# Performance work log

Hardware: AMD Instinct MI355X
Metric: run time of the kernel (lower is better)

## Reference

```python
import jax, jax.numpy as jnp
import numpy as np

B, T, D = 64, 8, 512          # batch, num_tokens (= num_heads), hidden_size (= head_dim)
S = 512                       # history seq_len
NKV = 4                       # num_key_value_heads
G = T // NKV                  # num_key_value_groups
EPS = 1e-6
SCALE = D ** -0.5
NEG_INF = float('-inf')


def rmsnorm(x, w):
    # Qwen3NextRMSNorm: norm in fp32, scale by (1 + weight), cast back
    xf = x.astype(jnp.float32)
    n = xf * jax.lax.rsqrt(jnp.mean(xf * xf, axis=-1, keepdims=True) + EPS)
    return (n * (1.0 + w.astype(jnp.float32))).astype(x.dtype)


def setup_inputs() -> dict:
    key = jax.random.key(0)
    ks = jax.random.split(key, 8)
    return {
        'target_emb': jax.random.normal(ks[0], (B, T, D), dtype=jnp.float32),
        'history_emb': jax.random.normal(ks[1], (B, S, D), dtype=jnp.float32),
        'key_padding_mask': jax.random.bernoulli(ks[2], 0.2, (B, S)),
        'q_proj_w': jax.random.normal(ks[3], (D, D), dtype=jnp.float32) * (D ** -0.5),
        'k_proj_w': jax.random.normal(ks[4], (NKV * D, D), dtype=jnp.float32) * (D ** -0.5),
        'v_proj_w': jax.random.normal(ks[5], (NKV * D, D), dtype=jnp.float32) * (D ** -0.5),
        'q_norm_w': jnp.zeros((D,), dtype=jnp.float32),
        'k_norm_w': jnp.zeros((D,), dtype=jnp.float32),
    }


def reference(target_emb, history_emb, key_padding_mask,
              q_proj_w, k_proj_w, v_proj_w, q_norm_w, k_norm_w):
    # q_proj on flattened tokens: [B,T,D] @ W^T -> [B,T,D]
    q = jnp.einsum('btd,ed->bte', target_emb, q_proj_w)
    q = rmsnorm(q, q_norm_w)
    # k/v projections: [B,S,D] -> [B,S,NKV,D]
    k = jnp.einsum('bsd,ed->bse', history_emb, k_proj_w).reshape(B, S, NKV, D)
    v = jnp.einsum('bsd,ed->bse', history_emb, v_proj_w).reshape(B, S, NKV, D)
    k = rmsnorm(k, k_norm_w)
    # group queries by kv head instead of materializing repeat_kv copies
    qg = q.reshape(B, NKV, G, D)              # [B,NKV,G,D]
    kt = jnp.transpose(k, (0, 2, 1, 3))        # [B,NKV,S,D]
    vt = jnp.transpose(v, (0, 2, 1, 3))        # [B,NKV,S,D]
    scores = jnp.einsum('bngd,bnsd->bngs', qg, kt) * SCALE  # [B,NKV,G,S]
    bias = jnp.where(key_padding_mask, NEG_INF, 0.0).astype(jnp.float32)
    scores = scores + bias[:, None, None, :]
    attn = jax.nn.softmax(scores.astype(jnp.float32), axis=-1).astype(q.dtype)
    out = jnp.einsum('bngs,bnsd->bngd', attn, vt)  # [B,NKV,G,D]
    tokens = out.reshape(B, T, D)
    attn_weights = attn.reshape(B, T, 1, S)       # matches torch [B,H,1,S]
    return (tokens, attn_weights)
```

## Files before the change

kernel.cpp:

```cpp
#include <hip/hip_runtime.h>
#include <stdint.h>

#define NB 64
#define NT 8
#define ND 512
#define NS 512
#define NKV 4
#define BSLICE 32
#define NSLICE (NB / BSLICE)

typedef __attribute__((ext_vector_type(8))) short short8_t;
typedef __attribute__((ext_vector_type(8))) unsigned short ushort8_t;
typedef __attribute__((ext_vector_type(4))) float f32x4;

typedef const __attribute__((address_space(1))) void gas_void;
typedef __attribute__((address_space(3))) void las_void;

#define HSP_HI 0ull
#define WKH_B  16777216ull
#define WVH_B  18874368ull
#define WKT_B  20971520ull
#define THI_B  23068672ull
#define TLO_B  23592960ull
#define QWH_B  24117248ull
#define QWL_B  24641536ull
#define QP_B   25165824ull
#define DOT_B  26214400ull
#define OUTF_B 27262976ull
#define SSQ_B  28311552ull
#define PBUF_B 28966912ull
#define QPF_B  31064064ull
#define HH_B   33161216ull
#define HL_B   33685504ull
#define FLAG_B 34209792ull
#define ZERO_CNT 917504

__device__ __forceinline__ float b2f(unsigned short u) {
    union { unsigned int i; float f; } x; x.i = ((unsigned int)u) << 16; return x.f;
}
__device__ __forceinline__ unsigned short f2b(float f) {
    union { float f; unsigned int i; } x; x.f = f;
    unsigned int i = x.i;
    unsigned int r = i + 0x7FFFu + ((i >> 16) & 1u);
    return (unsigned short)(r >> 16);
}
__device__ __forceinline__ float in_elem(const void* p, long long i, int is_f32) {
    return is_f32 ? ((const float*)p)[i] : b2f(((const unsigned short*)p)[i]);
}
__device__ __forceinline__ void store_out(void* out, int is_f32, size_t idx, float v) {
    if (is_f32) ((float*)out)[idx] = v;
    else        ((unsigned short*)out)[idx] = f2b(v);
}

__global__ __launch_bounds__(256) void scan_zero_kernel(const unsigned short* __restrict__ hraw,
                                                        const void* __restrict__ mraw,
                                                        int* __restrict__ flag,
                                                        float* __restrict__ zbase) {
    const int tid = threadIdx.x;
    const int bx = blockIdx.x;
    if (bx >= 2) {
        zbase[(size_t)(bx - 2) * 256 + tid] = 0.0f;
        return;
    }
    if (bx == 0) {
        __shared__ int cnt;
        if (tid == 0) cnt = 0;
        __syncthreads();
        int c = 0;
#pragma unroll
        for (int it = 0; it < 16; ++it) {
            unsigned int e = (hraw[tid + it * 256] >> 7) & 0xFFu;
            if (e >= 0xF0u) ++c;
        }
        if (c) atomicAdd(&cnt, c);
        __syncthreads();
        if (tid == 0) flag[0] = (cnt >= 8) ? 1 : 0;
    } else {
        __shared__ int s_bf16, s_f32, s_not01, s_oddnz;
        if (tid == 0) { s_bf16 = 0; s_f32 = 0; s_not01 = 0; s_oddnz = 0; }
        __syncthreads();
        const unsigned int* w32 = (const unsigned int*)mraw;
        int f_bf16 = 0, f_f32 = 0, f_not01 = 0, f_oddnz = 0;
#pragma unroll
        for (int it = 0; it < 32; ++it) {
            const int i = tid + it * 256;
            unsigned int w = w32[i];
            if (w == 0x00003F80u || w == 0x3F803F80u) f_bf16 = 1;
            if (w == 0x3F800000u) f_f32 = 1;
            if (w != 0u && w != 1u && w != 0x3F800000u) f_not01 = 1;
            if ((i & 1) && w != 0u) f_oddnz = 1;
        }
        if (f_bf16)  s_bf16 = 1;
        if (f_f32)   s_f32 = 1;
        if (f_not01) s_not01 = 1;
        if (f_oddnz) s_oddnz = 1;
        __syncthreads();
        if (tid == 0) {
            int mode;
            if (s_bf16)       mode = 3;
            else if (s_f32)   mode = 0;
            else if (s_not01) mode = 1;
            else if (s_oddnz) mode = 0;
            else              mode = 2;
            flag[1] = mode;
        }
    }
}

__device__ __forceinline__ void split8(const void* src, long long i8, int is_f32,
                                       ushort8_t& h, ushort8_t& l) {
    if (is_f32) {
        const float* s = (const float*)src + i8;
        float4 a = *(const float4*)s;
        float4 b = *(const float4*)(s + 4);
        float v[8] = {a.x, a.y, a.z, a.w, b.x, b.y, b.z, b.w};
#pragma unroll
        for (int j = 0; j < 8; ++j) {
            unsigned short hh = f2b(v[j]);
            h[j] = hh;
            l[j] = f2b(v[j] - b2f(hh));
        }
    } else {
        h = *(const ushort8_t*)((const unsigned short*)src + i8);
#pragma unroll
        for (int j = 0; j < 8; ++j) l[j] = 0;
    }
}
__device__ __forceinline__ ushort8_t hi8(const void* src, long long i8, int is_f32) {
    ushort8_t h;
    if (is_f32) {
        const float* s = (const float*)src + i8;
        float4 a = *(const float4*)s;
        float4 b = *(const float4*)(s + 4);
        float v[8] = {a.x, a.y, a.z, a.w, b.x, b.y, b.z, b.w};
#pragma unroll
        for (int j = 0; j < 8; ++j) h[j] = f2b(v[j]);
    } else {
        h = *(const ushort8_t*)((const unsigned short*)src + i8);
    }
    return h;
}

__global__ __launch_bounds__(256) void prep_kernel(const void* __restrict__ target,
                                                   const void* __restrict__ Wq,
                                                   const void* __restrict__ Wk,
                                                   const void* __restrict__ Wv,
                                                   unsigned short* __restrict__ tHi,
                                                   unsigned short* __restrict__ tLo,
                                                   unsigned short* __restrict__ qwHi,
                                                   unsigned short* __restrict__ qwLo,
                                                   unsigned short* __restrict__ wkHi,
                                                   unsigned short* __restrict__ wvHi,
                                                   const int* __restrict__ flag) {
    const int bx = blockIdx.x;
    const int tid = threadIdx.x;
    const int is_f32 = flag[0];
    if (bx < 128) {
        const long long i8 = ((long long)bx * 256 + tid) * 8;
        ushort8_t h, l;
        split8(target, i8, is_f32, h, l);
        *(ushort8_t*)(tHi + i8) = h;
        *(ushort8_t*)(tLo + i8) = l;
    } else if (bx < 256) {
        const long long i8 = ((long long)(bx - 128) * 256 + tid) * 8;
        ushort8_t h, l;
        split8(Wq, i8, is_f32, h, l);
        *(ushort8_t*)(qwHi + i8) = h;
        *(ushort8_t*)(qwLo + i8) = l;
    } else if (bx < 768) {
        const long long i8 = ((long long)(bx - 256) * 256 + tid) * 8;
        *(ushort8_t*)(wkHi + i8) = hi8(Wk, i8, is_f32);
    } else {
        const long long i8 = ((long long)(bx - 768) * 256 + tid) * 8;
        *(ushort8_t*)(wvHi + i8) = hi8(Wv, i8, is_f32);
    }
}

__global__ __launch_bounds__(256) void presplit_hist_kernel(const void* __restrict__ src,
                                                            unsigned short* __restrict__ hi,
                                                            const int* __restrict__ flag,
                                                            long long elemOff) {
    const long long i8 = ((long long)blockIdx.x * 256 + threadIdx.x) * 8;
    *(ushort8_t*)(hi + i8) = hi8(src, elemOff + i8, flag[0]);
}


__device__ __forceinline__ void mfma2_tile(const unsigned short* __restrict__ Ah,
                                           const unsigned short* __restrict__ Al,
                                           const unsigned short* __restrict__ B,
                                           unsigned short* AsH, unsigned short* AsL,
                                           unsigned short* Bs,
                                           int m0, int n0, int tid,
                                           int ktBeg, int ktEnd,
                                           f32x4 acc[4][4]) {
    const int lane = tid & 63, wave = tid >> 6;
    const int wr = wave >> 1, wc = wave & 1;
    const int lr = lane & 15, lq = lane >> 4;
#pragma unroll
    for (int i = 0; i < 4; ++i)
#pragma unroll
        for (int j = 0; j < 4; ++j) acc[i][j] = (f32x4){0.f, 0.f, 0.f, 0.f};

    for (int kt = ktBeg; kt < ktEnd; ++kt) {
        const int k0 = kt << 5;
#pragma unroll
        for (int i = 0; i < 2; ++i) {
            const int c = i * 256 + tid;
            const size_t aoff = (size_t)(m0 + (c >> 2)) * 512 + (k0 + (c & 3) * 8);
            const size_t boff = (size_t)(n0 + (c >> 2)) * 512 + (k0 + (c & 3) * 8);
            __builtin_amdgcn_global_load_lds((gas_void*)(Ah + aoff), (las_void*)(AsH + c * 8), 16, 0, 0);
            __builtin_amdgcn_global_load_lds((gas_void*)(Al + aoff), (las_void*)(AsL + c * 8), 16, 0, 0);
            __builtin_amdgcn_global_load_lds((gas_void*)(B + boff), (las_void*)(Bs + c * 8), 16, 0, 0);
        }
        __syncthreads();
        short8_t aH[4], aL[4], bF[4];
#pragma unroll
        for (int t = 0; t < 4; ++t) {
            const int ao = (wr * 64 + t * 16 + lr) * 32 + lq * 8;
            aH[t] = *(const short8_t*)(AsH + ao);
            aL[t] = *(const short8_t*)(AsL + ao);
            bF[t] = *(const short8_t*)(Bs + (wc * 64 + t * 16 + lr) * 32 + lq * 8);
        }
#pragma unroll
        for (int ti = 0; ti < 4; ++ti)
#pragma unroll
            for (int tj = 0; tj < 4; ++tj)
                acc[ti][tj] = __builtin_amdgcn_mfma_f32_16x16x32_bf16(aH[ti], bF[tj], acc[ti][tj], 0, 0, 0);
#pragma unroll
        for (int ti = 0; ti < 4; ++ti)
#pragma unroll
            for (int tj = 0; tj < 4; ++tj)
                acc[ti][tj] = __builtin_amdgcn_mfma_f32_16x16x32_bf16(aL[ti], bF[tj], acc[ti][tj], 0, 0, 0);
        __syncthreads();
    }
}

__device__ __forceinline__ void mfma3_tile(const unsigned short* __restrict__ Ah,
                                           const unsigned short* __restrict__ Al,
                                           const unsigned short* __restrict__ Bh,
                                           const unsigned short* __restrict__ Bl,
                                           unsigned short* AsH, unsigned short* AsL,
                                           unsigned short* BsH, unsigned short* BsL,
                                           int m0, int n0, int tid,
                                           int ktBeg, int ktEnd,
                                           f32x4 acc[4][4]) {
    const int lane = tid & 63, wave = tid >> 6;
    const int wr = wave >> 1, wc = wave & 1;
    const int lr = lane & 15, lq = lane >> 4;
#pragma unroll
    for (int i = 0; i < 4; ++i)
#pragma unroll
        for (int j = 0; j < 4; ++j) acc[i][j] = (f32x4){0.f, 0.f, 0.f, 0.f};

    for (int kt = ktBeg; kt < ktEnd; ++kt) {
        const int k0 = kt << 5;
#pragma unroll
        for (int i = 0; i < 2; ++i) {
            const int c = i * 256 + tid;
            const size_t aoff = (size_t)(m0 + (c >> 2)) * 512 + (k0 + (c & 3) * 8);
            const size_t boff = (size_t)(n0 + (c >> 2)) * 512 + (k0 + (c & 3) * 8);
            __builtin_amdgcn_global_load_lds((gas_void*)(Ah + aoff), (las_void*)(AsH + c * 8), 16, 0, 0);
            __builtin_amdgcn_global_load_lds((gas_void*)(Al + aoff), (las_void*)(AsL + c * 8), 16, 0, 0);
            __builtin_amdgcn_global_load_lds((gas_void*)(Bh + boff), (las_void*)(BsH + c * 8), 16, 0, 0);
            __builtin_amdgcn_global_load_lds((gas_void*)(Bl + boff), (las_void*)(BsL + c * 8), 16, 0, 0);
        }
        __syncthreads();
        short8_t aH[4], aL[4], bH[4], bL[4];
#pragma unroll
        for (int t = 0; t < 4; ++t) {
            const int ao = (wr * 64 + t * 16 + lr) * 32 + lq * 8;
            const int bo = (wc * 64 + t * 16 + lr) * 32 + lq * 8;
            aH[t] = *(const short8_t*)(AsH + ao);
            aL[t] = *(const short8_t*)(AsL + ao);
            bH[t] = *(const short8_t*)(BsH + bo);
            bL[t] = *(const short8_t*)(BsL + bo);
        }
#pragma unroll
        for (int ti = 0; ti < 4; ++ti)
#pragma unroll
            for (int tj = 0; tj < 4; ++tj)
                acc[ti][tj] = __builtin_amdgcn_mfma_f32_16x16x32_bf16(aH[ti], bH[tj], acc[ti][tj], 0, 0, 0);
#pragma unroll
    for (int ti = 0; ti < 4; ++ti)
#pragma unroll
            for (int tj = 0; tj < 4; ++tj)
                acc[ti][tj] = __builtin_amdgcn_mfma_f32_16x16x32_bf16(aH[ti], bL[tj], acc[ti][tj], 0, 0, 0);
#pragma unroll
        for (int ti = 0; ti < 4; ++ti)
#pragma unroll
            for (int tj = 0; tj < 4; ++tj)
                acc[ti][tj] = __builtin_amdgcn_mfma_f32_16x16x32_bf16(aL[ti], bH[tj], acc[ti][tj], 0, 0, 0);
        __syncthreads();
    }
}

__global__ __launch_bounds__(256) void gemm3_ks(const unsigned short* __restrict__ Ah,
                                                const unsigned short* __restrict__ Al,
                                                const unsigned short* __restrict__ Bh,
                                                const unsigned short* __restrict__ Bl,
                                                float* __restrict__ C) {
    __shared__ __align__(16) unsigned short AsH[128 * 32];
    __shared__ __align__(16) unsigned short AsL[128 * 32];
    __shared__ __align__(16) unsigned short BsH[128 * 32];
    __shared__ __align__(16) unsigned short BsL[128 * 32];
    const int m0 = blockIdx.x * 128, n0 = blockIdx.y * 128;
    const int kt0 = blockIdx.z * 4;
    const int tid = threadIdx.x;
    f32x4 acc[4][4];
    mfma3_tile(Ah, Al, Bh, Bl, AsH, AsL, BsH, BsL, m0, n0, tid, kt0, kt0 + 4, acc);
    const int lane = tid & 63, wave = tid >> 6;
    const int wr = wave >> 1, wc = wave & 1;
    const int lr = lane & 15, lq = lane >> 4;
#pragma unroll
    for (int ti = 0; ti < 4; ++ti)
#pragma unroll
        for (int tj = 0; tj < 4; ++tj)
#pragma unroll
            for (int r = 0; r < 4; ++r) {
                const int row = m0 + wr * 64 + ti * 16 + lq * 4 + r;
                const int col = n0 + wc * 64 + tj * 16 + lr;
                atomicAdd(&C[(size_t)row * 512 + col], acc[ti][tj][r]);
            }
}

__global__ __launch_bounds__(64) void rmsnorm_qperm(const float* __restrict__ q,
                                                    const void* __restrict__ qnw,
                                                    const void* __restrict__ knw,
                                                    float* __restrict__ qpF,
                                                    const int* __restrict__ flag) {
    const int row = blockIdx.x;
    const int lane = threadIdx.x;
    const int is_f32 = flag[0];
    const float* p = q + (size_t)row * ND + lane * 8;
    float v[8];
    float4 a = *(const float4*)p;
    float4 b4 = *(const float4*)(p + 4);
    v[0] = a.x; v[1] = a.y; v[2] = a.z; v[3] = a.w;
    v[4] = b4.x; v[5] = b4.y; v[6] = b4.z; v[7] = b4.w;
    float ssq = 0.f;
#pragma unroll
    for (int j = 0; j < 8; ++j) ssq = fmaf(v[j], v[j], ssq);
#pragma unroll
    for (int off = 1; off < 64; off <<= 1) ssq += __shfl_xor(ssq, off);
    float r = rsqrtf(ssq * (1.0f / ND) + 1e-6f);
    const float SCALE = 0.044194173824159216f;
    const int b = row >> 3, h = row & 7;
    const int prow = (h >> 1) * 128 + b * 2 + (h & 1);
    float o[8];
#pragma unroll
    for (int j = 0; j < 8; ++j) {
        int e = lane * 8 + j;
        o[j] = v[j] * r * (1.0f + in_elem(qnw, e, is_f32)) * (1.0f + in_elem(knw, e, is_f32)) * SCALE;
    }
    float4* dst = (float4*)(qpF + (size_t)prow * 512 + lane * 8);
    dst[0] = (float4){o[0], o[1], o[2], o[3]};
    dst[1] = (float4){o[4], o[5], o[6], o[7]};
}

#define SSQ8_ABUF(b) ((b) * 32768)
#define SSQ8_BBUF(b) (65536 + (b) * 32768)
#define EPI_STRIDE 136

#define SSQ8_STAGE_A(r, tt, bufOff)                                                       \
    do {                                                                                  \
        const int rcA0_ = rl0 + (r) * 64;                                                 \
        __builtin_amdgcn_global_load_lds(                                                 \
            (gas_void*)(A + (size_t)(mBase + rcA0_) * 512 + (tt) * 64 + ksw),             \
            (las_void*)(smem + (bufOff) + rcA0_ * 128 + k0 * 2), 16, 0, 0);               \
        const int rcA1_ = rcA0_ + 128;                                                    \
        __builtin_amdgcn_global_load_lds(                                                 \
            (gas_void*)(A + (size_t)(mBase + rcA1_) * 512 + (tt) * 64 + ksw),             \
            (las_void*)(smem + (bufOff) + rcA1_ * 128 + k0 * 2), 16, 0, 0);               \
    } while (0)

#define SSQ8_STAGE_B(q, tt, bufOff)                                                       \
    do {                                                                                  \
        const int rcB0_ = bR + (q) * 32;                                                  \
        __builtin_amdgcn_global_load_lds(                                                 \
            (gas_void*)(W + (size_t)(nBase + rcB0_) * 512 + (tt) * 64 + ksw),             \
            (las_void*)(smem + (bufOff) + rcB0_ * 128 + k0 * 2), 16, 0, 0);               \
        const int rcB1_ = rcB0_ + 128;                                                    \
        __builtin_amdgcn_global_load_lds(                                                 \
            (gas_void*)(W + (size_t)(nBase + rcB1_) * 512 + (tt) * 64 + ksw),             \
            (las_void*)(smem + (bufOff) + rcB1_ * 128 + k0 * 2), 16, 0, 0);               \
    } while (0)

#define SSQ8_READ_A(qm, bufOff)                                                           \
    _Pragma("unroll")                                                                     \
    for (int m_ = 0; m_ < 4; ++m_) {                                                      \
        const int rc_ = wm * 128 + (qm) * 64 + m_ * 16 + lr;                              \
        af[m_][0] = *(const short8_t*)(smem + (bufOff) + rc_ * 128 + kb0);                \
        af[m_][1] = *(const short8_t*)(smem + (bufOff) + rc_ * 128 + kb1);                \
    }

#define SSQ8_READ_B2(nh, bufOff)                                                          \
    _Pragma("unroll")                                                                     \
    for (int n_ = 0; n_ < 2; ++n_) {                                                      \
        const int cc_ = wn * 64 + (nh) * 32 + n_ * 16 + lr;                               \
        bf[(nh) * 2 + n_][0] = *(const short8_t*)(smem + (bufOff) + cc_ * 128 + kb0);     \
        bf[(nh) * 2 + n_][1] = *(const short8_t*)(smem + (bufOff) + cc_ * 128 + kb1);     \
    }

#define SSQ8_MFMA_Q(qm, nh)                                                               \
    _Pragma("unroll")                                                                     \
    for (int m_ = 0; m_ < 4; ++m_)                                                        \
    _Pragma("unroll")                                                                     \
    for (int n_ = 0; n_ < 2; ++n_) {                                                      \
        acc[(qm) * 4 + m_][(nh) * 2 + n_] = __builtin_amdgcn_mfma_f32_16x16x32_bf16(      \
            af[m_][0], bf[(nh) * 2 + n_][0], acc[(qm) * 4 + m_][(nh) * 2 + n_], 0, 0, 0); \
        acc[(qm) * 4 + m_][(nh) * 2 + n_] = __builtin_amdgcn_mfma_f32_16x16x32_bf16(      \
            af[m_][1], bf[(nh) * 2 + n_][1], acc[(qm) * 4 + m_][(nh) * 2 + n_], 0, 0, 0); \
    }

#define SSQ8_SYNC_PRE()                                                                   \
    __builtin_amdgcn_s_barrier();                                                         \
    asm volatile("s_waitcnt lgkmcnt(0)" ::: "memory");                                    \
    __builtin_amdgcn_sched_barrier(0);                                                    \
    __builtin_amdgcn_s_setprio(1);

#define SSQ8_SYNC_POST()                                                                  \
    __builtin_amdgcn_s_setprio(0);                                                        \
    __builtin_amdgcn_s_barrier();

__global__ __launch_bounds__(512) void gemm_ssq8(const unsigned short* __restrict__ A,
                                                 const unsigned short* __restrict__ W,
                                                 const float* __restrict__ qpF,
                                                 float* __restrict__ ssq,
                                                 float* __restrict__ dotb,
                                                 int b0) {
    extern __shared__ char smem[];
    const int tid = threadIdx.x;
    const int lane = tid & 63, wave = tid >> 6;
    const int wm = wave >> 2, wn = wave & 3;
    const int lr = lane & 15, lq = lane >> 4;
    const int mBase = blockIdx.x * 256;
    const int nBase = blockIdx.y * 256;

    const int rl0 = tid >> 3;
    const int k0 = (tid & 7) << 3;
    const int ksw = k0 ^ ((rl0 & 7) << 3);
    const int bR = (rl0 & 31) | ((rl0 >> 5) << 6);

    const int kb0 = ((lq * 8) ^ ((lr & 7) << 3)) * 2;
    const int kb1 = ((32 + lq * 8) ^ ((lr & 7) << 3)) * 2;

    f32x4 acc[8][4];
#pragma unroll
    for (int i = 0; i < 8; ++i)
#pragma unroll
        for (int j = 0; j < 4; ++j) acc[i][j] = (f32x4){0.f, 0.f, 0.f, 0.f};

    SSQ8_STAGE_A(0, 0, SSQ8_ABUF(0));
    SSQ8_STAGE_B(0, 0, SSQ8_BBUF(0));
    SSQ8_STAGE_A(1, 0, SSQ8_ABUF(0));
    SSQ8_STAGE_B(1, 0, SSQ8_BBUF(0));
    SSQ8_STAGE_A(0, 1, SSQ8_ABUF(1));
    SSQ8_STAGE_B(0, 1, SSQ8_BBUF(1));
    asm volatile("s_waitcnt vmcnt(4)" ::: "memory");
    __builtin_amdgcn_s_barrier();

    short8_t af[4][2], bf[4][2];

#pragma unroll
    for (int t = 0; t < 8; ++t) {
        const int cur = t & 1, nxt = cur ^ 1;
        const int aC = SSQ8_ABUF(cur), bC = SSQ8_BBUF(cur);
        const int aN = SSQ8_ABUF(nxt), bN = SSQ8_BBUF(nxt);
        SSQ8_READ_A(0, aC)
        SSQ8_READ_B2(0, bC)
        if (t + 1 < 8) SSQ8_STAGE_A(1, t + 1, aN);
        SSQ8_SYNC_PRE()
        SSQ8_MFMA_Q(0, 0)
        SSQ8_SYNC_POST()
        SSQ8_READ_B2(1, bC)
        if (t + 1 < 8) SSQ8_STAGE_B(1, t + 1, bN);
        SSQ8_SYNC_PRE()
        SSQ8_MFMA_Q(0, 1)
        SSQ8_SYNC_POST()
        SSQ8_READ_A(1, aC)
        if (t + 2 < 8) SSQ8_STAGE_A(0, t + 2, aC);
        SSQ8_SYNC_PRE()
        SSQ8_MFMA_Q(1, 0)
        SSQ8_SYNC_POST()
        if (t + 2 < 8) SSQ8_STAGE_B(0, t + 2, bC);
        __builtin_amdgcn_s_barrier();
        __builtin_amdgcn_sched_barrier(0);
        __builtin_amdgcn_s_setprio(1);
        SSQ8_MFMA_Q(1, 1)
        __builtin_amdgcn_s_setprio(0);
        if (t < 6) {
            asm volatile("s_waitcnt vmcnt(4)" ::: "memory");
        } else if (t == 6) {
            asm volatile("s_waitcnt vmcnt(0)" ::: "memory");
        }
        __builtin_amdgcn_s_barrier();
    }

    const int nh = (int)(blockIdx.y >> 1);
    const int bG = b0 + (mBase >> 9);
    const int bn = bG * 4 + nh;
    const int sBase0 = mBase & 511;
    const int dBase = (nBase & 511) + wn * 64 + lr;
    const size_t qrow0 = (size_t)(nh * 128 + bG * 2) * 512;
    float qv0[4], qv1[4];
#pragma unroll
    for (int n = 0; n < 4; ++n) {
        qv0[n] = qpF[qrow0 + dBase + n * 16];
        qv1[n] = qpF[qrow0 + 512 + dBase + n * 16];
    }
    float* lv   = (float*)smem;
    float* ld0  = lv  + 64 * EPI_STRIDE;
    float* ld1  = ld0 + 64 * EPI_STRIDE;
    float* part = ld1 + 64 * EPI_STRIDE;
    const int col = wn * 16 + lr;

#pragma unroll
    for (int p = 0; p < 2; ++p) {
        __syncthreads();
#pragma unroll
        for (int mm = 0; mm < 4; ++mm) {
            const int m = p * 4 + mm;
            f32x4 vv, dd0, dd1;
#pragma unroll
            for (int r = 0; r < 4; ++r) {
                float v = 0.f, d0 = 0.f, d1 = 0.f;
#pragma unroll
                for (int n = 0; n < 4; ++n) {
                    float x = acc[m][n][r];
                    v = fmaf(x, x, v);
                    d0 = fmaf(x, qv0[n], d0);
                    d1 = fmaf(x, qv1[n], d1);
                }
                vv[r] = v; dd0[r] = d0; dd1[r] = d1;
            }
            const int idx = wm * 64 + mm * 16 + lq * 4;
            *(f32x4*)(lv  + col * EPI_STRIDE + idx) = vv;
            *(f32x4*)(ld0 + col * EPI_STRIDE + idx) = dd0;
            *(f32x4*)(ld1 + col * EPI_STRIDE + idx) = dd1;
        }
        __syncthreads();
        {
            const int t = tid >> 7, i = tid & 127;
            float s0 = 0.f, s1 = 0.f, s2 = 0.f;
#pragma unroll
            for (int c = 0; c < 16; ++c) {
                const int cc = t * 16 + c;
                s0 += lv [cc * EPI_STRIDE + i];
                s1 += ld0[cc * EPI_STRIDE + i];
                s2 += ld1[cc * EPI_STRIDE + i];
            }
            part[(0 * 128 + i) * 4 + t] = s0;
            part[(1 * 128 + i) * 4 + t] = s1;
            part[(2 * 128 + i) * 4 + t] = s2;
        }
        __syncthreads();
        if (tid < 384) {
            const int v = tid >> 7, i = tid & 127;
            f32x4 pp = *(const f32x4*)(part + ((size_t)v * 128 + i) * 4);
            float sum = (pp[0] + pp[1]) + (pp[2] + pp[3]);
            const int s = sBase0 + (i >> 6) * 128 + p * 64 + (i & 63);
            if (v == 0)      atomicAdd(&ssq[(size_t)bn * 512 + s], sum);
            else if (v == 1) atomicAdd(&dotb[((size_t)bn * 2 + 0) * 512 + s], sum);
            else             atomicAdd(&dotb[((size_t)bn * 2 + 1) * 512 + s], sum);
        }
    }
}

__global__ __launch_bounds__(512) void softmax_slice(const float* __restrict__ ssq,
                                                     const float* __restrict__ dot,
                                                     const void* __restrict__ mraw,
                                                     float* __restrict__ pbuf,
                                                     void* __restrict__ out,
                                                     const int* __restrict__ flag,
                                                     int b0) {
    const int bn = b0 * 4 + blockIdx.x;
    const int b = bn >> 2;
    const int tid = threadIdx.x;
    const int wave = tid >> 6, lane = tid & 63;
    const int is_f32 = flag[0];
    const int mode = flag[1];
    __shared__ float red[32];

    float sq = ssq[(size_t)bn * 512 + tid];
    float rms = rsqrtf(sq * (1.0f / ND) + 1e-6f);
    const int mi = b * NS + tid;
    int masked;
    if (mode == 3)      masked = (((const unsigned short*)mraw)[mi] != 0);
    else if (mode == 1) masked = (((const unsigned char*)mraw)[mi] != 0);
    else if (mode == 0) masked = (((const unsigned int*)mraw)[mi] != 0u);
    else                masked = (((const unsigned int*)mraw)[2 * mi] != 0u);
    float ninf = -__builtin_inff();
    float v0 = masked ? ninf : dot[((size_t)bn * 2 + 0) * 512 + tid] * rms;
    float v1 = masked ? ninf : dot[((size_t)bn * 2 + 1) * 512 + tid] * rms;

    float m0 = v0, m1 = v1;
#pragma unroll
    for (int off = 1; off < 64; off <<= 1) {
        m0 = fmaxf(m0, __shfl_xor(m0, off));
        m1 = fmaxf(m1, __shfl_xor(m1, off));
    }
    if (lane == 0) { red[wave] = m0; red[8 + wave] = m1; }
    __syncthreads();
    m0 = red[0]; m1 = red[8];
#pragma unroll
    for (int w = 1; w < 8; ++w) { m0 = fmaxf(m0, red[w]); m1 = fmaxf(m1, red[8 + w]); }
    float e0 = __expf(v0 - m0), e1 = __expf(v1 - m1);
    float su0 = e0, su1 = e1;
#pragma unroll
    for (int off = 1; off < 64; off <<= 1) {
        su0 += __shfl_xor(su0, off);
        su1 += __shfl_xor(su1, off);
    }
    if (lane == 0) { red[16 + wave] = su0; red[24 + wave] = su1; }
    __syncthreads();
    float t0 = 0.f, t1 = 0.f;
#pragma unroll
    for (int w = 0; w < 8; ++w) { t0 += red[16 + w]; t1 += red[24 + w]; }
    float p0 = e0 / t0, p1 = e1 / t1;

    pbuf[((size_t)bn * 2 + 0) * 512 + tid] = p0;
    pbuf[((size_t)bn * 2 + 1) * 512 + tid] = p1;
    size_t abase = 262144u + (size_t)bn * 1024 + tid;
    store_out(out, is_f32, abase, p0);
    store_out(out, is_f32, abase + 512, p1);
}

__global__ __launch_bounds__(512) void htilde_kernel(const unsigned short* __restrict__ hspHi,
                                                     const float* __restrict__ pbuf,
                                                     unsigned short* __restrict__ hHi,
                                                     unsigned short* __restrict__ hLo,
                                                     int b0) {
    __shared__ float pl[8][512];
    __shared__ float red[8][64][8];
    const int bl = blockIdx.x;
    const int bG = b0 + bl;
    const int d0 = blockIdx.y * 64;
    const int tid = threadIdx.x;
#pragma unroll
    for (int k = 0; k < 8; ++k) {
        const int j = tid + k * 512;
        const int h = j >> 9, s = j & 511;
        pl[h][s] = pbuf[((size_t)(bG * 4 + (h >> 1)) * 2 + (h & 1)) * 512 + s];
    }
    __syncthreads();

    const int dl = tid & 63, sl = tid >> 6;
    const unsigned short* hb = hspHi + (size_t)bl * 512 * 512 + d0 + dl;
    float acc[8];
#pragma unroll
    for (int h = 0; h < 8; ++h) acc[h] = 0.f;
#pragma unroll 4
    for (int i = 0; i < 64; ++i) {
        const int s = i * 8 + sl;
        float hv = b2f(hb[(size_t)s * 512]);
#pragma unroll
        for (int h = 0; h < 8; ++h) acc[h] = fmaf(pl[h][s], hv, acc[h]);
    }
#pragma unroll
    for (int h = 0; h < 8; ++h) red[sl][dl][h] = acc[h];
    __syncthreads();

    const int dl2 = tid >> 3, h2 = tid & 7;
    float v = 0.f;
#pragma unroll
    for (int s2 = 0; s2 < 8; ++s2) v += red[s2][dl2][h2];
    const int row = (h2 >> 1) * 128 + bG * 2 + (h2 & 1);
    unsigned short hv = f2b(v);
    hHi[(size_t)row * 512 + d0 + dl2] = hv;
    hLo[(size_t)row * 512 + d0 + dl2] = f2b(v - b2f(hv));
}

__global__ __launch_bounds__(256) void gemm_out_ks(const unsigned short* __restrict__ hHi,
                                                   const unsigned short* __restrict__ hLo,
                                                   const unsigned short* __restrict__ wvHi,
                                                   float* __restrict__ outF) {
    __shared__ __align__(16) unsigned short AsH[128 * 32];
    __shared__ __align__(16) unsigned short AsL[128 * 32];
    __shared__ __align__(16) unsigned short Bs[128 * 32];
    const int n = blockIdx.x;
    const int m0 = n * 128, n0 = blockIdx.y * 128;
    const int kt0 = blockIdx.z * 4;
    const int tid = threadIdx.x;
    f32x4 acc[4][4];
    mfma2_tile(hHi, hLo, wvHi + (size_t)n * 512 * 512, AsH, AsL, Bs, m0, n0, tid, kt0, kt0 + 4, acc);

    const int lane = tid & 63, wave = tid >> 6;
    const int wr = wave >> 1, wc = wave & 1;
    const int lr = lane & 15, lq = lane >> 4;
#pragma unroll
    for (int ti = 0; ti < 4; ++ti)
#pragma unroll
        for (int tj = 0; tj < 4; ++tj)
#pragma unroll
            for (int r = 0; r < 4; ++r) {
                const int row = m0 + wr * 64 + ti * 16 + lq * 4 + r;
                const int e = n0 + wc * 64 + tj * 16 + lr;
                atomicAdd(&outF[(size_t)row * 512 + e], acc[ti][tj][r]);
            }
}

__global__ __launch_bounds__(256) void out_final_kernel(const float* __restrict__ outF,
                                                        void* __restrict__ out,
                                                        const int* __restrict__ flag) {
    const size_t i = (size_t)blockIdx.x * 256 + threadIdx.x;
    const int row = (int)(i >> 9), e = (int)(i & 511);
    const int n = row >> 7, rl = row & 127;
    const int b = rl >> 1, g = rl & 1;
    store_out(out, flag[0], (size_t)(b * 8 + n * 2 + g) * 512 + e, outF[i]);
}

extern "C" void kernel_launch(void* const* d_in, const int* in_sizes, int n_in,
                              void* d_out, int out_size, void* d_ws, size_t ws_size,
                              hipStream_t stream) {
    (void)in_sizes; (void)n_in; (void)out_size; (void)ws_size;
    const void* target = d_in[0];
    const void* hist   = d_in[1];
    const void* mraw   = d_in[2];
    const void* Wq     = d_in[3];
    const void* Wk     = d_in[4];
    const void* Wv     = d_in[5];
    const void* qnw    = d_in[6];
    const void* knw    = d_in[7];

    char* w = (char*)d_ws;
    unsigned short* hspHi = (unsigned short*)(w + HSP_HI);
    unsigned short* wkHi  = (unsigned short*)(w + WKH_B);
    unsigned short* wvHi  = (unsigned short*)(w + WVH_B);
    unsigned short* tHi   = (unsigned short*)(w + THI_B);
    unsigned short* tLo   = (unsigned short*)(w + TLO_B);
    unsigned short* qwHi  = (unsigned short*)(w + QWH_B);
    unsigned short* qwLo  = (unsigned short*)(w + QWL_B);
    float* qp    = (float*)(w + QP_B);
    float* dotb  = (float*)(w + DOT_B);
    float* outF  = (float*)(w + OUTF_B);
    float* ssq   = (float*)(w + SSQ_B);
    float* pbuf  = (float*)(w + PBUF_B);
    float* qpF   = (float*)(w + QPF_B);
    unsigned short* hHi  = (unsigned short*)(w + HH_B);
    unsigned short* hLo  = (unsigned short*)(w + HL_B);
    int* flag = (int*)(w + FLAG_B);

    static bool attr_set = false;
    if (!attr_set) {
        (void)hipFuncSetAttribute(reinterpret_cast<const void*>(&gemm_ssq8),
                                  hipFuncAttributeMaxDynamicSharedMemorySize, 131072);
        attr_set = true;
    }

    scan_zero_kernel<<<2 + ZERO_CNT / 256, 256, 0, stream>>>(
        (const unsigned short*)hist, mraw, flag, qp);
    prep_kernel<<<1280, 256, 0, stream>>>(target, Wq, Wk, Wv, tHi, tLo, qwHi, qwLo,
                                          wkHi, wvHi, flag);

    gemm3_ks<<<dim3(4, 4, 4), 256, 0, stream>>>(tHi, tLo, qwHi, qwLo, qp);
    rmsnorm_qperm<<<NB * NT, 64, 0, stream>>>(qp, qnw, knw, qpF, flag);

    for (int sl = 0; sl < NSLICE; ++sl) {
        const int b0 = sl * BSLICE;
        presplit_hist_kernel<<<4096, 256, 0, stream>>>(hist, hspHi, flag,
                                                       (long long)sl * BSLICE * 512 * 512);
        gemm_ssq8<<<dim3(64, 8), 512, 131072, stream>>>(hspHi, wkHi, qpF, ssq, dotb, b0);
        softmax_slice<<<BSLICE * NKV, 512, 0, stream>>>(ssq, dotb, mraw, pbuf, d_out, flag, b0);
        htilde_kernel<<<dim3(BSLICE, 8), 512, 0, stream>>>(hspHi, pbuf, hHi, hLo, b0);
    }
    gemm_out_ks<<<dim3(4, 4, 4), 256, 0, stream>>>(hHi, hLo, wvHi, outF);
    out_final_kernel<<<1024, 256, 0, stream>>>(outF, d_out, flag);
}
```

Before: 244.7 us.

## Fuse history bf16 conversion into GEMM A-staging and htilde loads

Removes the separate presplit_hist kernel that converted history embeddings to bf16 in workspace. The GEMM now loads fp32 (or bf16) history directly into registers, converts it, and writes it to LDS through a software-pipelined register stage in place of direct global-to-LDS loads. htilde reads the raw fp32 history directly. This saves one kernel launch per slice and a write plus re-read of the bf16 copy. In exchange the GEMM reads twice the bytes for A, uses more registers, and its load pipeline and waitcnt accounting become more complex.

```diff
diff --git a/kernel.cpp b/kernel.cpp
--- a/kernel.cpp
+++ b/kernel.cpp
@@ -176,14 +176,6 @@
     }
 }
 
-__global__ __launch_bounds__(256) void presplit_hist_kernel(const void* __restrict__ src,
-                                                            unsigned short* __restrict__ hi,
-                                                            const int* __restrict__ flag,
-                                                            long long elemOff) {
-    const long long i8 = ((long long)blockIdx.x * 256 + threadIdx.x) * 8;
-    *(ushort8_t*)(hi + i8) = hi8(src, elemOff + i8, flag[0]);
-}
-
 
 __device__ __forceinline__ void mfma2_tile(const unsigned short* __restrict__ Ah,
                                            const unsigned short* __restrict__ Al,
@@ -361,16 +353,31 @@
 #define SSQ8_BBUF(b) (65536 + (b) * 32768)
 #define EPI_STRIDE 136
 
-#define SSQ8_STAGE_A(r, tt, bufOff)                                                       \
+#define SSQA_ISSUE(r0, r1, tt, F, U)                                                      \
     do {                                                                                  \
-        const int rcA0_ = rl0 + (r) * 64;                                                 \
-        __builtin_amdgcn_global_load_lds(                                                 \
-            (gas_void*)(A + (size_t)(mBase + rcA0_) * 512 + (tt) * 64 + ksw),             \
-            (las_void*)(smem + (bufOff) + rcA0_ * 128 + k0 * 2), 16, 0, 0);               \
-        const int rcA1_ = rcA0_ + 128;                                                    \
-        __builtin_amdgcn_global_load_lds(                                                 \
-            (gas_void*)(A + (size_t)(mBase + rcA1_) * 512 + (tt) * 64 + ksw),             \
-            (las_void*)(smem + (bufOff) + rcA1_ * 128 + k0 * 2), 16, 0, 0);               \
+        const size_t ke_ = (size_t)(tt) * 64 + ksw;                                       \
+        if (is_f32) {                                                                     \
+            F[0] = *(const float4*)(histF + (size_t)(mBase + (r0)) * 512 + ke_);          \
+            F[1] = *(const float4*)(histF + (size_t)(mBase + (r0)) * 512 + ke_ + 4);      \
+            F[2] = *(const float4*)(histF + (size_t)(mBase + (r1)) * 512 + ke_);          \
+            F[3] = *(const float4*)(histF + (size_t)(mBase + (r1)) * 512 + ke_ + 4);      \
+        } else {                                                                          \
+            U[0] = *(const ushort8_t*)(histU + (size_t)(mBase + (r0)) * 512 + ke_);       \
+            U[1] = *(const ushort8_t*)(histU + (size_t)(mBase + (r1)) * 512 + ke_);       \
+        }                                                                                 \
+    } while (0)
+
+#define SSQA_WRITE(r0, r1, bufOff, F, U)                                                  \
+    do {                                                                                  \
+        ushort8_t w0_, w1_;                                                               \
+        if (is_f32) {                                                                     \
+            float v0_[8] = {F[0].x, F[0].y, F[0].z, F[0].w, F[1].x, F[1].y, F[1].z, F[1].w}; \
+            float v1_[8] = {F[2].x, F[2].y, F[2].z, F[2].w, F[3].x, F[3].y, F[3].z, F[3].w}; \
+            _Pragma("unroll")                                                             \
+            for (int j_ = 0; j_ < 8; ++j_) { w0_[j_] = (short)f2b(v0_[j_]); w1_[j_] = (short)f2b(v1_[j_]); } \
+        } else { w0_ = (ushort8_t)U[0]; w1_ = (ushort8_t)U[1]; }                          \
+        *(ushort8_t*)(smem + (bufOff) + (r0) * 128 + k0 * 2) = w0_;                       \
+        *(ushort8_t*)(smem + (bufOff) + (r1) * 128 + k0 * 2) = w1_;                       \
     } while (0)
 
 #define SSQ8_STAGE_B(q, tt, bufOff)                                                       \
@@ -422,11 +429,12 @@
     __builtin_amdgcn_s_setprio(0);                                                        \
     __builtin_amdgcn_s_barrier();
 
-__global__ __launch_bounds__(512) void gemm_ssq8(const unsigned short* __restrict__ A,
+__global__ __launch_bounds__(512) void gemm_ssq8(const void* __restrict__ hist,
                                                  const unsigned short* __restrict__ W,
                                                  const float* __restrict__ qpF,
                                                  float* __restrict__ ssq,
                                                  float* __restrict__ dotb,
+                                                 const int* __restrict__ flag,
                                                  int b0) {
     extern __shared__ char smem[];
     const int tid = threadIdx.x;
@@ -435,11 +443,18 @@
     const int lr = lane & 15, lq = lane >> 4;
     const int mBase = blockIdx.x * 256;
     const int nBase = blockIdx.y * 256;
+    const int is_f32 = flag[0];
+
+    const size_t sliceOff = (size_t)b0 * 512 * 512;
+    const float* histF = (const float*)hist + sliceOff;
+    const unsigned short* histU = (const unsigned short*)hist + sliceOff;
 
     const int rl0 = tid >> 3;
     const int k0 = (tid & 7) << 3;
     const int ksw = k0 ^ ((rl0 & 7) << 3);
     const int bR = (rl0 & 31) | ((rl0 >> 5) << 6);
+    const int arE0 = rl0, arE1 = rl0 + 128;
+    const int arO0 = rl0 + 64, arO1 = rl0 + 192;
 
     const int kb0 = ((lq * 8) ^ ((lr & 7) << 3)) * 2;
     const int kb1 = ((32 + lq * 8) ^ ((lr & 7) << 3)) * 2;
@@ -450,13 +465,21 @@
 #pragma unroll
         for (int j = 0; j < 4; ++j) acc[i][j] = (f32x4){0.f, 0.f, 0.f, 0.f};
 
-    SSQ8_STAGE_A(0, 0, SSQ8_ABUF(0));
+    float4 fE[4], fO[4];
+    ushort8_t uE[2], uO[2];
+
+    SSQA_ISSUE(arE0, arE1, 0, fE, uE);
+    SSQA_ISSUE(arO0, arO1, 0, fO, uO);
     SSQ8_STAGE_B(0, 0, SSQ8_BBUF(0));
-    SSQ8_STAGE_A(1, 0, SSQ8_ABUF(0));
     SSQ8_STAGE_B(1, 0, SSQ8_BBUF(0));
-    SSQ8_STAGE_A(0, 1, SSQ8_ABUF(1));
     SSQ8_STAGE_B(0, 1, SSQ8_BBUF(1));
-    asm volatile("s_waitcnt vmcnt(4)" ::: "memory");
+    SSQA_WRITE(arE0, arE1, SSQ8_ABUF(0), fE, uE);
+    SSQA_WRITE(arO0, arO1, SSQ8_ABUF(0), fO, uO);
+    SSQA_ISSUE(arE0, arE1, 1, fE, uE);
+    SSQA_WRITE(arE0, arE1, SSQ8_ABUF(1), fE, uE);
+    SSQA_ISSUE(arO0, arO1, 1, fO, uO);
+    asm volatile("s_waitcnt lgkmcnt(0)" ::: "memory");
+    __builtin_amdgcn_sched_barrier(0);
     __builtin_amdgcn_s_barrier();
 
     short8_t af[4][2], bf[4][2];
@@ -468,7 +491,8 @@
         const int aN = SSQ8_ABUF(nxt), bN = SSQ8_BBUF(nxt);
         SSQ8_READ_A(0, aC)
         SSQ8_READ_B2(0, bC)
-        if (t + 1 < 8) SSQ8_STAGE_A(1, t + 1, aN);
+        if (t < 7) SSQA_WRITE(arO0, arO1, aN, fO, uO);
+        if (t < 6) SSQA_ISSUE(arE0, arE1, t + 2, fE, uE);
         SSQ8_SYNC_PRE()
         SSQ8_MFMA_Q(0, 0)
         SSQ8_SYNC_POST()
@@ -478,7 +502,7 @@
         SSQ8_MFMA_Q(0, 1)
         SSQ8_SYNC_POST()
         SSQ8_READ_A(1, aC)
-        if (t + 2 < 8) SSQ8_STAGE_A(0, t + 2, aC);
+        if (t < 6) { SSQA_WRITE(arE0, arE1, aC, fE, uE); SSQA_ISSUE(arO0, arO1, t + 2, fO, uO); }
         SSQ8_SYNC_PRE()
         SSQ8_MFMA_Q(1, 0)
         SSQ8_SYNC_POST()
@@ -489,7 +513,8 @@
         SSQ8_MFMA_Q(1, 1)
         __builtin_amdgcn_s_setprio(0);
         if (t < 6) {
-            asm volatile("s_waitcnt vmcnt(4)" ::: "memory");
+            if (is_f32) { asm volatile("s_waitcnt vmcnt(6)" ::: "memory"); }
+            else        { asm volatile("s_waitcnt vmcnt(4)" ::: "memory"); }
         } else if (t == 6) {
             asm volatile("s_waitcnt vmcnt(0)" ::: "memory");
         }
@@ -625,10 +650,11 @@
     store_out(out, is_f32, abase + 512, p1);
 }
 
-__global__ __launch_bounds__(512) void htilde_kernel(const unsigned short* __restrict__ hspHi,
+__global__ __launch_bounds__(512) void htilde_kernel(const void* __restrict__ hist,
                                                      const float* __restrict__ pbuf,
                                                      unsigned short* __restrict__ hHi,
                                                      unsigned short* __restrict__ hLo,
+                                                     const int* __restrict__ flag,
                                                      int b0) {
     __shared__ float pl[8][512];
     __shared__ float red[8][64][8];
@@ -636,6 +662,7 @@
     const int bG = b0 + bl;
     const int d0 = blockIdx.y * 64;
     const int tid = threadIdx.x;
+    const int is_f32 = flag[0];
 #pragma unroll
     for (int k = 0; k < 8; ++k) {
         const int j = tid + k * 512;
@@ -645,16 +672,28 @@
     __syncthreads();
 
     const int dl = tid & 63, sl = tid >> 6;
-    const unsigned short* hb = hspHi + (size_t)bl * 512 * 512 + d0 + dl;
+    const size_t hbase = (size_t)bG * 262144 + (size_t)(d0 + dl);
     float acc[8];
 #pragma unroll
     for (int h = 0; h < 8; ++h) acc[h] = 0.f;
+    if (is_f32) {
+        const float* hF = (const float*)hist + hbase;
 #pragma unroll 4
-    for (int i = 0; i < 64; ++i) {
-        const int s = i * 8 + sl;
-        float hv = b2f(hb[(size_t)s * 512]);
-#pragma unroll
-        for (int h = 0; h < 8; ++h) acc[h] = fmaf(pl[h][s], hv, acc[h]);
+        for (int i = 0; i < 64; ++i) {
+            const int s = i * 8 + sl;
+            float hv = hF[(size_t)s * 512];
+#pragma unroll
+            for (int h = 0; h < 8; ++h) acc[h] = fmaf(pl[h][s], hv, acc[h]);
+        }
+    } else {
+        const unsigned short* hU = (const unsigned short*)hist + hbase;
+#pragma unroll 4
+        for (int i = 0; i < 64; ++i) {
+            const int s = i * 8 + sl;
+            float hv = b2f(hU[(size_t)s * 512]);
+#pragma unroll
+            for (int h = 0; h < 8; ++h) acc[h] = fmaf(pl[h][s], hv, acc[h]);
+        }
     }
 #pragma unroll
     for (int h = 0; h < 8; ++h) red[sl][dl][h] = acc[h];
@@ -723,7 +762,6 @@
     const void* knw    = d_in[7];
 
     char* w = (char*)d_ws;
-    unsigned short* hspHi = (unsigned short*)(w + HSP_HI);
     unsigned short* wkHi  = (unsigned short*)(w + WKH_B);
     unsigned short* wvHi  = (unsigned short*)(w + WVH_B);
     unsigned short* tHi   = (unsigned short*)(w + THI_B);
@@ -757,11 +795,9 @@
 
     for (int sl = 0; sl < NSLICE; ++sl) {
         const int b0 = sl * BSLICE;
-        presplit_hist_kernel<<<4096, 256, 0, stream>>>(hist, hspHi, flag,
-                                                       (long long)sl * BSLICE * 512 * 512);
-        gemm_ssq8<<<dim3(64, 8), 512, 131072, stream>>>(hspHi, wkHi, qpF, ssq, dotb, b0);
+        gemm_ssq8<<<dim3(64, 8), 512, 131072, stream>>>(hist, wkHi, qpF, ssq, dotb, flag, b0);
         softmax_slice<<<BSLICE * NKV, 512, 0, stream>>>(ssq, dotb, mraw, pbuf, d_out, flag, b0);
-        htilde_kernel<<<dim3(BSLICE, 8), 512, 0, stream>>>(hspHi, pbuf, hHi, hLo, b0);
+        htilde_kernel<<<dim3(BSLICE, 8), 512, 0, stream>>>(hist, pbuf, hHi, hLo, flag, b0);
     }
     gemm_out_ks<<<dim3(4, 4, 4), 256, 0, stream>>>(hHi, hLo, wvHi, outF);
     out_final_kernel<<<1024, 256, 0, stream>>>(outF, d_out, flag);
```

After: 433.8 us. +77.3%, slower.
